# Kernel tuning notes

Hardware: AMD Instinct MI355X
Metric: run time of the kernel (lower is better)

The kernel has to match this reference:

```python
import jax, jax.numpy as jnp
import numpy as np

B = 2048   # batch size
D = 2048   # feature dim (ResNet-50)
H = 2048   # projection hidden dim
T = 0.1    # temperature
EPS_BN = 1e-5
CC_ITERS = 32  # >= ~2*log2(B), enough for pointer-jumping convergence


def setup_inputs() -> dict:
    key = jax.random.key(0)
    ks = jax.random.split(key, 4)
    s = 0.02
    return {
        "x1": jax.random.normal(ks[0], (B, D), dtype=jnp.float32),
        "x2": jax.random.normal(ks[1], (B, D), dtype=jnp.float32),
        "W1": jax.random.normal(ks[2], (H, D), dtype=jnp.float32) * s,
        "b1": jnp.zeros((H,), jnp.float32),
        "gamma": jnp.ones((H,), jnp.float32),
        "beta": jnp.zeros((H,), jnp.float32),
        "W2": jax.random.normal(ks[3], (D, H), dtype=jnp.float32) * s,
        "b2": jnp.zeros((D,), jnp.float32),
    }


def _head(x, W1, b1, gamma, beta, W2, b2):
    # ProjectionHead: Linear -> BatchNorm1d (train mode, batch stats) -> ReLU -> Linear
    h = x @ W1.T + b1
    mu = h.mean(0)
    var = h.var(0)  # biased variance, as torch BN uses for normalization
    h = (h - mu) * jax.lax.rsqrt(var + EPS_BN) * gamma + beta
    h = jax.nn.relu(h)
    o = h @ W2.T + b2
    n = jnp.maximum(jnp.linalg.norm(o, axis=1, keepdims=True), 1e-12)
    return o / n  # F.normalize


def _cc_mask(feat):
    # build_connected_component: kNN(k=1) graph + connected components -> same-label mask
    b = feat.shape[0]
    sim = jax.lax.stop_gradient(feat @ feat.T) - 2.0 * jnp.eye(b, dtype=feat.dtype)
    y = jnp.argmax(sim, axis=1)  # topk(1) neighbor per row
    # min-label propagation with pointer jumping (GPU-native union-find equivalent)
    def body(_, l):
        ln = jnp.minimum(l, l[y])      # propagate along edge i -> y[i]
        ln = ln.at[y].min(l)           # propagate along reverse edge y[i] -> i
        return jnp.minimum(ln, ln[ln])  # pointer jumping
    labels = jax.lax.fori_loop(0, CC_ITERS, body, jnp.arange(b))
    return (labels[:, None] == labels[None, :]).astype(feat.dtype)


def _sup_contra(logits, mask, diag):
    dm = 1.0 - diag
    mask = mask * dm
    exp_logits = jnp.exp(logits) * dm
    log_prob = logits - jnp.log(exp_logits.sum(1, keepdims=True))
    mean_log_prob_pos = (mask * log_prob).sum(1) / mask.sum(1)
    return (-mean_log_prob_pos).mean()


def reference(x1, x2, W1, b1, gamma, beta, W2, b2):
    # Only head2 branch contributes to the returned graph_loss (head1 branch is dead code
    # w.r.t. the return value), so we compute exactly the graph_loss path.
    feat1 = _head(x1, W1, b1, gamma, beta, W2, b2)
    feat2 = _head(x2, W1, b1, gamma, beta, W2, b2)
    mask1 = _cc_mask(feat1)
    mask2 = _cc_mask(feat2)
    diag = jnp.eye(B, dtype=feat1.dtype)
    loss = _sup_contra(feat1 @ feat1.T / T, mask2, diag)
    loss = loss + _sup_contra(feat2 @ feat2.T / T, mask1, diag)
    return loss / 2.0
```

## Files before the change

### kernel.cpp

```cpp
#include <hip/hip_runtime.h>
#include <hip/hip_bf16.h>

typedef __bf16 bf16_t;
typedef __bf16 bf16x4 __attribute__((ext_vector_type(4)));
typedef __bf16 bf16x8 __attribute__((ext_vector_type(8)));
typedef float  f32x4  __attribute__((ext_vector_type(4)));

__device__ __forceinline__ void gload_lds16(const void* g, void* l)
{
    __builtin_amdgcn_global_load_lds((__attribute__((address_space(1))) void*)g,
                                     (__attribute__((address_space(3))) void*)l,
                                     16, 0, 0);
}

__global__ __launch_bounds__(256) void cast_all(const float* __restrict__ x1, const float* __restrict__ x2,
                                                const float* __restrict__ W1, const float* __restrict__ W2,
                                                bf16_t* __restrict__ xcatb, bf16_t* __restrict__ W1b,
                                                bf16_t* __restrict__ W2b)
{
    const size_t i  = ((size_t)blockIdx.x * 256 + threadIdx.x) * 4;
    const size_t M4 = 1ull << 22;
    const size_t r  = i >> 22;
    const size_t off = i & (M4 - 1);
    const float* src; bf16_t* dst;
    if (r == 0)      { src = x1; dst = xcatb; }
    else if (r == 1) { src = x2; dst = xcatb + M4; }
    else if (r == 2) { src = W1; dst = W1b; }
    else             { src = W2; dst = W2b; }
    f32x4 v = *(const f32x4*)(src + off);
    bf16x4 o;
    o[0] = (bf16_t)v[0]; o[1] = (bf16_t)v[1]; o[2] = (bf16_t)v[2]; o[3] = (bf16_t)v[3];
    *(bf16x4*)(dst + off) = o;
}

__global__ __launch_bounds__(256) void gemm_bt(
    const bf16_t* __restrict__ A, const bf16_t* __restrict__ B,
    const float* __restrict__ bias, void* __restrict__ Cv,
    int N, int K, int rows_per_batch, long long b_batch_stride,
    int mode, int c_bf16,
    float* __restrict__ ps, float* __restrict__ ps2,
    float* __restrict__ rsq, const float* __restrict__ rnv,
    unsigned long long* __restrict__ pkey)
{
    __shared__ bf16_t lsA[128 * 64];
    __shared__ bf16_t lsB[128 * 64];
    __shared__ float  cs2[4][64];
    __shared__ float  cq2[4][64];
    __shared__ float  rq2[4][64];
    __shared__ unsigned long long kv2[4][64];
    const int tid  = threadIdx.x;
    const int lane = tid & 63;
    const int wave = tid >> 6;
    const int wm   = (wave >> 1) * 64;
    const int wn   = (wave & 1) * 64;
    const int m0   = blockIdx.y * 128;
    const int n0   = blockIdx.x * 128;
    const bf16_t* Bb = B + (long long)(m0 / rows_per_batch) * b_batch_stride;

    f32x4 acc[4][4] = {};

    const int srow = tid >> 3;
    const int scol = (tid & 7) * 8;
    for (int kt = 0; kt < K; kt += 64) {
#pragma unroll
        for (int i = 0; i < 4; ++i) {
            const int r = i * 32 + srow;
            gload_lds16(A  + (size_t)(m0 + r) * K + kt + scol, lsA + r * 64 + scol);
            gload_lds16(Bb + (size_t)(n0 + r) * K + kt + scol, lsB + r * 64 + scol);
        }
        __syncthreads();
#pragma unroll
        for (int ks = 0; ks < 2; ++ks) {
            const int kk = ks * 32 + (lane >> 4) * 8;
            bf16x8 af[4], bfr[4];
#pragma unroll
            for (int f = 0; f < 4; ++f) {
                af[f]  = *(const bf16x8*)&lsA[(wm + f * 16 + (lane & 15)) * 64 + kk];
                bfr[f] = *(const bf16x8*)&lsB[(wn + f * 16 + (lane & 15)) * 64 + kk];
            }
#pragma unroll
            for (int fm = 0; fm < 4; ++fm)
#pragma unroll
                for (int fn = 0; fn < 4; ++fn)
                    acc[fm][fn] = __builtin_amdgcn_mfma_f32_16x16x32_bf16(af[fm], bfr[fn], acc[fm][fn], 0, 0, 0);
        }
        __syncthreads();
    }

    if (mode == 2) {
        const int rnb = (m0 >> 11) * 2048;
#pragma unroll
        for (int fm = 0; fm < 4; ++fm) {
            const int mb = m0 + wm + fm * 16 + ((lane >> 4) << 2);
            const f32x4 rm = *(const f32x4*)&rnv[mb];
#pragma unroll
            for (int fn = 0; fn < 4; ++fn) {
                const float rc = rnv[rnb + n0 + wn + fn * 16 + (lane & 15)];
#pragma unroll
                for (int r = 0; r < 4; ++r)
                    acc[fm][fn][r] *= rm[r] * rc;
            }
        }
    }

#pragma unroll
    for (int fm = 0; fm < 4; ++fm) {
        const int rb = m0 + wm + fm * 16 + ((lane >> 4) << 2);
#pragma unroll
        for (int fn = 0; fn < 4; ++fn) {
            const int colg = n0 + wn + fn * 16 + (lane & 15);
            const float bv = bias ? bias[colg] : 0.0f;
            if (c_bf16) {
                bf16_t* Cb = (bf16_t*)Cv;
#pragma unroll
                for (int r = 0; r < 4; ++r)
                    Cb[(size_t)(rb + r) * N + colg] = (bf16_t)(acc[fm][fn][r] + bv);
            } else {
                float* Cf = (float*)Cv;
#pragma unroll
                for (int r = 0; r < 4; ++r)
                    Cf[(size_t)(rb + r) * N + colg] = acc[fm][fn][r] + bv;
            }
        }
    }

    if (mode == 1) {
#pragma unroll
        for (int fn = 0; fn < 4; ++fn) {
            const int cl = fn * 16 + (lane & 15);
            const float bv = bias[n0 + wn + cl];
            float s = 0.f, q = 0.f;
#pragma unroll
            for (int fm = 0; fm < 4; ++fm)
#pragma unroll
                for (int r = 0; r < 4; ++r) {
                    const float v = acc[fm][fn][r] + bv;
                    s += v; q += v * v;
                }
            s += __shfl_xor(s, 16); q += __shfl_xor(q, 16);
            s += __shfl_xor(s, 32); q += __shfl_xor(q, 32);
            if (lane < 16) { cs2[wave][cl] = s; cq2[wave][cl] = q; }
        }
        __syncthreads();
        if (tid < 128) {
            const int wlo = (tid < 64) ? 0 : 1;
            const int cl  = tid & 63;
            ps [(size_t)blockIdx.y * 2048 + n0 + tid] = cs2[wlo][cl] + cs2[wlo + 2][cl];
            ps2[(size_t)blockIdx.y * 2048 + n0 + tid] = cq2[wlo][cl] + cq2[wlo + 2][cl];
        }
    } else if (mode == 3) {
#pragma unroll
        for (int fm = 0; fm < 4; ++fm)
#pragma unroll
            for (int r = 0; r < 4; ++r) {
                float q = 0.f;
#pragma unroll
                for (int fn = 0; fn < 4; ++fn) {
                    const float v = acc[fm][fn][r] + bias[n0 + wn + fn * 16 + (lane & 15)];
                    q += v * v;
                }
                q += __shfl_xor(q, 1); q += __shfl_xor(q, 2);
                q += __shfl_xor(q, 4); q += __shfl_xor(q, 8);
                if ((lane & 15) == 0)
                    rq2[wave][fm * 16 + ((lane >> 4) << 2) + r] = q;
            }
        __syncthreads();
        if (tid < 128) {
            const int wlo = (tid < 64) ? 0 : 2;
            const int rl  = tid & 63;
            rsq[(size_t)blockIdx.x * 4096 + m0 + tid] = rq2[wlo][rl] + rq2[wlo + 1][rl];
        }
    } else if (mode == 2) {
#pragma unroll
        for (int fm = 0; fm < 4; ++fm)
#pragma unroll
            for (int r = 0; r < 4; ++r) {
                const int rl   = fm * 16 + ((lane >> 4) << 2) + r;
                const int self = (m0 + wm + rl) & 2047;
                float best = -1.0e38f; int bi = 0x7fffffff;
#pragma unroll
                for (int fn = 0; fn < 4; ++fn) {
                    const int cg = n0 + wn + fn * 16 + (lane & 15);
                    const float v = acc[fm][fn][r];
                    if (cg != self && v > best) { best = v; bi = cg; }
                }
#pragma unroll
                for (int st = 1; st <= 8; st <<= 1) {
                    const float ov = __shfl_xor(best, st);
                    const int   oi = __shfl_xor(bi, st);
                    if (ov > best || (ov == best && oi < bi)) { best = ov; bi = oi; }
                }
                if ((lane & 15) == 0) {
                    unsigned u = __float_as_uint(best);
                    u = (u & 0x80000000u) ? ~u : (u | 0x80000000u);
                    kv2[wave][rl] = ((unsigned long long)u << 32) | (unsigned)(~bi);
                }
            }
        __syncthreads();
        if (tid < 128) {
            const int wlo = (tid < 64) ? 0 : 2;
            const int rl  = tid & 63;
            const unsigned long long a = kv2[wlo][rl], b = kv2[wlo + 1][rl];
            pkey[(size_t)blockIdx.x * 4096 + m0 + tid] = a > b ? a : b;
        }
    }
}

__global__ __launch_bounds__(256) void bn_final2(const float* __restrict__ ps, const float* __restrict__ ps2,
                                                 float* __restrict__ mu, float* __restrict__ rinv)
{
    const int c = blockIdx.x * 256 + threadIdx.x;
    const int b = c >> 11, col = c & 2047;
    float s = 0.f, s2 = 0.f;
    for (int i = 0; i < 16; ++i) {
        s  += ps [(size_t)(b * 16 + i) * 2048 + col];
        s2 += ps2[(size_t)(b * 16 + i) * 2048 + col];
    }
    const float m = s * (1.0f / 2048.0f);
    const float v = s2 * (1.0f / 2048.0f) - m * m;
    mu[c]   = m;
    rinv[c] = rsqrtf(v + 1e-5f);
}

__global__ __launch_bounds__(256) void bn_apply(const bf16_t* __restrict__ h, const float* __restrict__ mu,
                                                const float* __restrict__ rinv, const float* __restrict__ gamma,
                                                const float* __restrict__ beta, bf16_t* __restrict__ out)
{
    const size_t base = ((size_t)blockIdx.x * 256 + threadIdx.x) * 8;
    const int col = (int)(base & 2047);
    const int br  = (int)(base >> 22);
    bf16x8 v = *(const bf16x8*)(h + base);
    bf16x8 o;
#pragma unroll
    for (int j = 0; j < 8; ++j) {
        const int c = col + j;
        const float f = (float)v[j];
        const float t = (f - mu[br * 2048 + c]) * rinv[br * 2048 + c] * gamma[c] + beta[c];
        o[j] = (bf16_t)fmaxf(t, 0.0f);
    }
    *(bf16x8*)(out + base) = o;
}

__global__ __launch_bounds__(256) void norm_final(const float* __restrict__ rsq, float* __restrict__ rn)
{
    const int r = blockIdx.x * 256 + threadIdx.x;
    float s = 0.f;
    for (int nb = 0; nb < 16; ++nb) s += rsq[(size_t)nb * 4096 + r];
    rn[r] = 1.0f / fmaxf(sqrtf(s), 1e-12f);
}

__global__ __launch_bounds__(1024) void cc_labels(const unsigned long long* __restrict__ pkey,
                                                  int* __restrict__ labg)
{
    __shared__ int A_[2048];
    __shared__ int Bn[2048];
    __shared__ int Y_[2048];
    __shared__ int chg;
    const int br = blockIdx.x;
    const int t = threadIdx.x;
    if (t == 0) chg = 0;
    for (int i = t; i < 2048; i += 1024) {
        const int row = br * 2048 + i;
        unsigned long long k = 0ull;
        for (int nb = 0; nb < 16; ++nb) {
            const unsigned long long v = pkey[(size_t)nb * 4096 + row];
            k = (v > k) ? v : k;
        }
        Y_[i] = (int)~((unsigned)(k & 0xFFFFFFFFull));
        A_[i] = i;
    }
    __syncthreads();
    for (int it = 0; it < 32; ++it) {
        for (int i = t; i < 2048; i += 1024) Bn[i] = min(A_[i], A_[Y_[i]]);
        __syncthreads();
        for (int i = t; i < 2048; i += 1024) atomicMin(&Bn[Y_[i]], A_[i]);
        __syncthreads();
        int ch = 0;
        for (int i = t; i < 2048; i += 1024) {
            const int b = Bn[i];
            const int nv = min(b, Bn[b]);
            if (nv != A_[i]) { ch = 1; A_[i] = nv; }
        }
        if (ch) atomicOr(&chg, 1);
        __syncthreads();
        const int c = chg;
        __syncthreads();
        if (t == 0) chg = 0;
        if (!c) break;
    }
    for (int i = t; i < 2048; i += 1024) labg[br * 2048 + i] = A_[i];
}

__global__ __launch_bounds__(256) void loss_rows(const float* __restrict__ sim, const int* __restrict__ labels,
                                                 float* __restrict__ terms)
{
    const int row = blockIdx.x;
    const int br  = row >> 11;
    const int* lab = labels + ((1 - br) << 11);
    const int self = row & 2047;
    const int li = lab[self];
    const int t = threadIdx.x;
    const f32x4* p = (const f32x4*)(sim + (size_t)row * 2048);
    f32x4 a = p[t * 2], b = p[t * 2 + 1];
    float se = 0.f, psum = 0.f; int pc = 0;
#pragma unroll
    for (int j = 0; j < 8; ++j) {
        const int c = t * 8 + j;
        const float v = (j < 4) ? a[j] : b[j - 4];
        if (c == self) continue;
        const float lg = v * 10.0f;
        se += expf(lg);
        if (lab[c] == li) { psum += lg; pc++; }
    }
    __shared__ float SE[256], PS[256]; __shared__ int PC[256];
    SE[t] = se; PS[t] = psum; PC[t] = pc;
    __syncthreads();
    for (int off = 128; off; off >>= 1) {
        if (t < off) { SE[t] += SE[t + off]; PS[t] += PS[t + off]; PC[t] += PC[t + off]; }
        __syncthreads();
    }
    if (t == 0) terms[row] = logf(SE[0]) - PS[0] / (float)PC[0];
}

__global__ __launch_bounds__(1024) void final_reduce(const float* __restrict__ terms, float* __restrict__ out)
{
    const int t = threadIdx.x;
    float s = terms[t] + terms[t + 1024] + terms[t + 2048] + terms[t + 3072];
    __shared__ float S[1024];
    S[t] = s;
    __syncthreads();
    for (int off = 512; off; off >>= 1) { if (t < off) S[t] += S[t + off]; __syncthreads(); }
    if (t == 0) out[0] = S[0] * (1.0f / 4096.0f);
}

extern "C" void kernel_launch(void* const* d_in, const int* in_sizes, int n_in,
                              void* d_out, int out_size, void* d_ws, size_t ws_size,
                              hipStream_t stream)
{
    const float* x1    = (const float*)d_in[0];
    const float* x2    = (const float*)d_in[1];
    const float* W1    = (const float*)d_in[2];
    const float* b1    = (const float*)d_in[3];
    const float* gamma = (const float*)d_in[4];
    const float* beta  = (const float*)d_in[5];
    const float* W2    = (const float*)d_in[6];
    const float* b2    = (const float*)d_in[7];

    char* ws = (char*)d_ws;
    const size_t MB = 1024ull * 1024ull;
    const size_t NN = 2048ull * 2048ull;
    bf16_t* W1b    = (bf16_t*)(ws + 0);
    bf16_t* W2b    = (bf16_t*)(ws + 8 * MB);
    bf16_t* xcatb  = (bf16_t*)(ws + 16 * MB);
    bf16_t* hnb    = (bf16_t*)(ws + 16 * MB);
    bf16_t* hb16   = (bf16_t*)(ws + 32 * MB);
    bf16_t* ob16   = (bf16_t*)(ws + 64 * MB);
    float*  sim    = (float*)(ws + 0);
    float*  psA    = (float*)(ws + 80 * MB);
    float*  psB    = psA + 32 * 2048;
    float*  rsq    = psB + 32 * 2048;
    float*  mu     = rsq + 16 * 4096;
    float*  rinv   = mu + 4096;
    float*  rn     = rinv + 4096;
    unsigned long long* pkey = (unsigned long long*)(rn + 4096);
    int*    labels = (int*)(pkey + 16 * 4096);
    float*  terms  = (float*)(labels + 4096);

    cast_all<<<16384, 256, 0, stream>>>(x1, x2, W1, W2, xcatb, W1b, W2b);

    gemm_bt<<<dim3(16, 32), 256, 0, stream>>>(xcatb, W1b, b1, hb16, 2048, 2048, 1 << 30, 0,
                                              1, 1, psA, psB, nullptr, nullptr, nullptr);
    bn_final2<<<16, 256, 0, stream>>>(psA, psB, mu, rinv);
    bn_apply<<<4096, 256, 0, stream>>>(hb16, mu, rinv, gamma, beta, hnb);

    gemm_bt<<<dim3(16, 32), 256, 0, stream>>>(hnb, W2b, b2, ob16, 2048, 2048, 1 << 30, 0,
                                              3, 1, nullptr, nullptr, rsq, nullptr, nullptr);
    norm_final<<<16, 256, 0, stream>>>(rsq, rn);

    gemm_bt<<<dim3(16, 32), 256, 0, stream>>>(ob16, ob16, nullptr, sim, 2048, 2048, 2048, (long long)NN,
                                              2, 0, nullptr, nullptr, nullptr, rn, pkey);

    cc_labels<<<2, 1024, 0, stream>>>(pkey, labels);
    loss_rows<<<4096, 256, 0, stream>>>(sim, labels, terms);
    final_reduce<<<1, 1024, 0, stream>>>(terms, (float*)d_out);
}
```

Measured before the change: 231.4 us.

## Use 8-wave GEMM tiles, fuse softmax exp-sum into sim GEMM, store sim as bf16

The GEMM now runs 512 threads (8 waves, each owning a 64x32 subtile) on the same 128x128 block tile, so each wave holds fewer accumulators. The similarity GEMM epilogue now computes per-row partial sums of exp(10*sim) alongside the argmax and writes them to a new partial buffer. Because of that, the sim matrix can be stored in bf16 and loss_rows only reads it for the positive-mask sum, which halves that matrix's memory traffic. The exp-sum is computed from fp32 accumulators, but the positive log-prob sum now reads bf16-rounded values, which slightly lowers precision.

```diff
diff --git a/kernel.cpp b/kernel.cpp
--- a/kernel.cpp
+++ b/kernel.cpp
@@ -33,38 +33,39 @@
     *(bf16x4*)(dst + off) = o;
 }
 
-__global__ __launch_bounds__(256) void gemm_bt(
+__global__ __launch_bounds__(512, 4) void gemm_bt(
     const bf16_t* __restrict__ A, const bf16_t* __restrict__ B,
     const float* __restrict__ bias, void* __restrict__ Cv,
     int N, int K, int rows_per_batch, long long b_batch_stride,
     int mode, int c_bf16,
     float* __restrict__ ps, float* __restrict__ ps2,
     float* __restrict__ rsq, const float* __restrict__ rnv,
-    unsigned long long* __restrict__ pkey)
+    unsigned long long* __restrict__ pkey, float* __restrict__ lseP)
 {
     __shared__ bf16_t lsA[128 * 64];
     __shared__ bf16_t lsB[128 * 64];
-    __shared__ float  cs2[4][64];
-    __shared__ float  cq2[4][64];
-    __shared__ float  rq2[4][64];
-    __shared__ unsigned long long kv2[4][64];
+    __shared__ float  cs2[8][32];
+    __shared__ float  cq2[8][32];
+    __shared__ float  rq2[8][64];
+    __shared__ float  ls2[8][64];
+    __shared__ unsigned long long kv2[8][64];
     const int tid  = threadIdx.x;
     const int lane = tid & 63;
     const int wave = tid >> 6;
-    const int wm   = (wave >> 1) * 64;
-    const int wn   = (wave & 1) * 64;
+    const int wm   = (wave >> 2) * 64;
+    const int wn   = (wave & 3) * 32;
     const int m0   = blockIdx.y * 128;
     const int n0   = blockIdx.x * 128;
     const bf16_t* Bb = B + (long long)(m0 / rows_per_batch) * b_batch_stride;
 
-    f32x4 acc[4][4] = {};
+    f32x4 acc[4][2] = {};
 
     const int srow = tid >> 3;
     const int scol = (tid & 7) * 8;
     for (int kt = 0; kt < K; kt += 64) {
 #pragma unroll
-        for (int i = 0; i < 4; ++i) {
-            const int r = i * 32 + srow;
+        for (int i = 0; i < 2; ++i) {
+            const int r = i * 64 + srow;
             gload_lds16(A  + (size_t)(m0 + r) * K + kt + scol, lsA + r * 64 + scol);
             gload_lds16(Bb + (size_t)(n0 + r) * K + kt + scol, lsB + r * 64 + scol);
         }
@@ -72,16 +73,17 @@
 #pragma unroll
         for (int ks = 0; ks < 2; ++ks) {
             const int kk = ks * 32 + (lane >> 4) * 8;
-            bf16x8 af[4], bfr[4];
-#pragma unroll
-            for (int f = 0; f < 4; ++f) {
+            bf16x8 af[4], bfr[2];
+#pragma unroll
+            for (int f = 0; f < 4; ++f)
                 af[f]  = *(const bf16x8*)&lsA[(wm + f * 16 + (lane & 15)) * 64 + kk];
-                bfr[f] = *(const bf16x8*)&lsB[(wn + f * 16 + (lane & 15)) * 64 + kk];
-            }
+#pragma unroll
+            for (int g = 0; g < 2; ++g)
+                bfr[g] = *(const bf16x8*)&lsB[(wn + g * 16 + (lane & 15)) * 64 + kk];
 #pragma unroll
             for (int fm = 0; fm < 4; ++fm)
 #pragma unroll
-                for (int fn = 0; fn < 4; ++fn)
+                for (int fn = 0; fn < 2; ++fn)
                     acc[fm][fn] = __builtin_amdgcn_mfma_f32_16x16x32_bf16(af[fm], bfr[fn], acc[fm][fn], 0, 0, 0);
         }
         __syncthreads();
@@ -94,7 +96,7 @@
             const int mb = m0 + wm + fm * 16 + ((lane >> 4) << 2);
             const f32x4 rm = *(const f32x4*)&rnv[mb];
 #pragma unroll
-            for (int fn = 0; fn < 4; ++fn) {
+            for (int fn = 0; fn < 2; ++fn) {
                 const float rc = rnv[rnb + n0 + wn + fn * 16 + (lane & 15)];
 #pragma unroll
                 for (int r = 0; r < 4; ++r)
@@ -107,7 +109,7 @@
     for (int fm = 0; fm < 4; ++fm) {
         const int rb = m0 + wm + fm * 16 + ((lane >> 4) << 2);
 #pragma unroll
-        for (int fn = 0; fn < 4; ++fn) {
+        for (int fn = 0; fn < 2; ++fn) {
             const int colg = n0 + wn + fn * 16 + (lane & 15);
             const float bv = bias ? bias[colg] : 0.0f;
             if (c_bf16) {
@@ -126,9 +128,9 @@
 
     if (mode == 1) {
 #pragma unroll
-        for (int fn = 0; fn < 4; ++fn) {
-            const int cl = fn * 16 + (lane & 15);
-            const float bv = bias[n0 + wn + cl];
+        for (int fn = 0; fn < 2; ++fn) {
+            const int cl32 = fn * 16 + (lane & 15);
+            const float bv = bias[n0 + wn + cl32];
             float s = 0.f, q = 0.f;
 #pragma unroll
             for (int fm = 0; fm < 4; ++fm)
@@ -139,14 +141,13 @@
                 }
             s += __shfl_xor(s, 16); q += __shfl_xor(q, 16);
             s += __shfl_xor(s, 32); q += __shfl_xor(q, 32);
-            if (lane < 16) { cs2[wave][cl] = s; cq2[wave][cl] = q; }
+            if (lane < 16) { cs2[wave][cl32] = s; cq2[wave][cl32] = q; }
         }
         __syncthreads();
         if (tid < 128) {
-            const int wlo = (tid < 64) ? 0 : 1;
-            const int cl  = tid & 63;
-            ps [(size_t)blockIdx.y * 2048 + n0 + tid] = cs2[wlo][cl] + cs2[wlo + 2][cl];
-            ps2[(size_t)blockIdx.y * 2048 + n0 + tid] = cq2[wlo][cl] + cq2[wlo + 2][cl];
+            const int qv = tid >> 5, cl = tid & 31;
+            ps [(size_t)blockIdx.y * 2048 + n0 + tid] = cs2[qv][cl] + cs2[qv + 4][cl];
+            ps2[(size_t)blockIdx.y * 2048 + n0 + tid] = cq2[qv][cl] + cq2[qv + 4][cl];
         }
     } else if (mode == 3) {
 #pragma unroll
@@ -155,7 +156,7 @@
             for (int r = 0; r < 4; ++r) {
                 float q = 0.f;
 #pragma unroll
-                for (int fn = 0; fn < 4; ++fn) {
+                for (int fn = 0; fn < 2; ++fn) {
                     const float v = acc[fm][fn][r] + bias[n0 + wn + fn * 16 + (lane & 15)];
                     q += v * v;
                 }
@@ -166,9 +167,9 @@
             }
         __syncthreads();
         if (tid < 128) {
-            const int wlo = (tid < 64) ? 0 : 2;
-            const int rl  = tid & 63;
-            rsq[(size_t)blockIdx.x * 4096 + m0 + tid] = rq2[wlo][rl] + rq2[wlo + 1][rl];
+            const int wlo = (tid >> 6) * 4, rl = tid & 63;
+            rsq[(size_t)blockIdx.x * 4096 + m0 + tid] =
+                rq2[wlo][rl] + rq2[wlo + 1][rl] + rq2[wlo + 2][rl] + rq2[wlo + 3][rl];
         }
     } else if (mode == 2) {
 #pragma unroll
@@ -177,31 +178,39 @@
             for (int r = 0; r < 4; ++r) {
                 const int rl   = fm * 16 + ((lane >> 4) << 2) + r;
                 const int self = (m0 + wm + rl) & 2047;
-                float best = -1.0e38f; int bi = 0x7fffffff;
-#pragma unroll
-                for (int fn = 0; fn < 4; ++fn) {
+                float best = -1.0e38f; int bi = 0x7fffffff; float se = 0.f;
+#pragma unroll
+                for (int fn = 0; fn < 2; ++fn) {
                     const int cg = n0 + wn + fn * 16 + (lane & 15);
                     const float v = acc[fm][fn][r];
-                    if (cg != self && v > best) { best = v; bi = cg; }
+                    if (cg != self) {
+                        se += expf(10.0f * v);
+                        if (v > best) { best = v; bi = cg; }
+                    }
                 }
 #pragma unroll
                 for (int st = 1; st <= 8; st <<= 1) {
                     const float ov = __shfl_xor(best, st);
                     const int   oi = __shfl_xor(bi, st);
                     if (ov > best || (ov == best && oi < bi)) { best = ov; bi = oi; }
+                    se += __shfl_xor(se, st);
                 }
                 if ((lane & 15) == 0) {
                     unsigned u = __float_as_uint(best);
                     u = (u & 0x80000000u) ? ~u : (u | 0x80000000u);
                     kv2[wave][rl] = ((unsigned long long)u << 32) | (unsigned)(~bi);
+                    ls2[wave][rl] = se;
                 }
             }
         __syncthreads();
         if (tid < 128) {
-            const int wlo = (tid < 64) ? 0 : 2;
-            const int rl  = tid & 63;
-            const unsigned long long a = kv2[wlo][rl], b = kv2[wlo + 1][rl];
-            pkey[(size_t)blockIdx.x * 4096 + m0 + tid] = a > b ? a : b;
+            const int wlo = (tid >> 6) * 4, rl = tid & 63;
+            unsigned long long k = kv2[wlo][rl];
+#pragma unroll
+            for (int j = 1; j < 4; ++j) { const unsigned long long v = kv2[wlo + j][rl]; k = v > k ? v : k; }
+            pkey[(size_t)blockIdx.x * 4096 + m0 + tid] = k;
+            lseP[(size_t)blockIdx.x * 4096 + m0 + tid] =
+                ls2[wlo][rl] + ls2[wlo + 1][rl] + ls2[wlo + 2][rl] + ls2[wlo + 3][rl];
         }
     }
 }
@@ -291,8 +300,8 @@
     for (int i = t; i < 2048; i += 1024) labg[br * 2048 + i] = A_[i];
 }
 
-__global__ __launch_bounds__(256) void loss_rows(const float* __restrict__ sim, const int* __restrict__ labels,
-                                                 float* __restrict__ terms)
+__global__ __launch_bounds__(256) void loss_rows(const bf16_t* __restrict__ simb, const int* __restrict__ labels,
+                                                 const float* __restrict__ lseP, float* __restrict__ terms)
 {
     const int row = blockIdx.x;
     const int br  = row >> 11;
@@ -300,26 +309,26 @@
     const int self = row & 2047;
     const int li = lab[self];
     const int t = threadIdx.x;
-    const f32x4* p = (const f32x4*)(sim + (size_t)row * 2048);
-    f32x4 a = p[t * 2], b = p[t * 2 + 1];
-    float se = 0.f, psum = 0.f; int pc = 0;
+    const bf16x8 v8 = *(const bf16x8*)(simb + (size_t)row * 2048 + t * 8);
+    float psum = 0.f; int pc = 0;
 #pragma unroll
     for (int j = 0; j < 8; ++j) {
         const int c = t * 8 + j;
-        const float v = (j < 4) ? a[j] : b[j - 4];
         if (c == self) continue;
-        const float lg = v * 10.0f;
-        se += expf(lg);
-        if (lab[c] == li) { psum += lg; pc++; }
-    }
-    __shared__ float SE[256], PS[256]; __shared__ int PC[256];
-    SE[t] = se; PS[t] = psum; PC[t] = pc;
+        if (lab[c] == li) { psum += 10.0f * (float)v8[j]; pc++; }
+    }
+    __shared__ float PS[256]; __shared__ int PC[256];
+    PS[t] = psum; PC[t] = pc;
     __syncthreads();
     for (int off = 128; off; off >>= 1) {
-        if (t < off) { SE[t] += SE[t + off]; PS[t] += PS[t + off]; PC[t] += PC[t + off]; }
-        __syncthreads();
-    }
-    if (t == 0) terms[row] = logf(SE[0]) - PS[0] / (float)PC[0];
+        if (t < off) { PS[t] += PS[t + off]; PC[t] += PC[t + off]; }
+        __syncthreads();
+    }
+    if (t == 0) {
+        float se = 0.f;
+        for (int nb = 0; nb < 16; ++nb) se += lseP[(size_t)nb * 4096 + row];
+        terms[row] = logf(se) - PS[0] / (float)PC[0];
+    }
 }
 
 __global__ __launch_bounds__(1024) void final_reduce(const float* __restrict__ terms, float* __restrict__ out)
@@ -355,32 +364,33 @@
     bf16_t* hnb    = (bf16_t*)(ws + 16 * MB);
     bf16_t* hb16   = (bf16_t*)(ws + 32 * MB);
     bf16_t* ob16   = (bf16_t*)(ws + 64 * MB);
-    float*  sim    = (float*)(ws + 0);
+    bf16_t* simb   = (bf16_t*)(ws + 0);
     float*  psA    = (float*)(ws + 80 * MB);
     float*  psB    = psA + 32 * 2048;
     float*  rsq    = psB + 32 * 2048;
     float*  mu     = rsq + 16 * 4096;
     float*  rinv   = mu + 4096;
     float*  rn     = rinv + 4096;
-    unsigned long long* pkey = (unsigned long long*)(rn + 4096);
+    float*  lseP   = rn + 4096;
+    unsigned long long* pkey = (unsigned long long*)(lseP + 16 * 4096);
     int*    labels = (int*)(pkey + 16 * 4096);
     float*  terms  = (float*)(labels + 4096);
 
     cast_all<<<16384, 256, 0, stream>>>(x1, x2, W1, W2, xcatb, W1b, W2b);
 
-    gemm_bt<<<dim3(16, 32), 256, 0, stream>>>(xcatb, W1b, b1, hb16, 2048, 2048, 1 << 30, 0,
-                                              1, 1, psA, psB, nullptr, nullptr, nullptr);
+    gemm_bt<<<dim3(16, 32), 512, 0, stream>>>(xcatb, W1b, b1, hb16, 2048, 2048, 1 << 30, 0,
+                                              1, 1, psA, psB, nullptr, nullptr, nullptr, nullptr);
     bn_final2<<<16, 256, 0, stream>>>(psA, psB, mu, rinv);
     bn_apply<<<4096, 256, 0, stream>>>(hb16, mu, rinv, gamma, beta, hnb);
 
-    gemm_bt<<<dim3(16, 32), 256, 0, stream>>>(hnb, W2b, b2, ob16, 2048, 2048, 1 << 30, 0,
-                                              3, 1, nullptr, nullptr, rsq, nullptr, nullptr);
+    gemm_bt<<<dim3(16, 32), 512, 0, stream>>>(hnb, W2b, b2, ob16, 2048, 2048, 1 << 30, 0,
+                                              3, 1, nullptr, nullptr, rsq, nullptr, nullptr, nullptr);
     norm_final<<<16, 256, 0, stream>>>(rsq, rn);
 
-    gemm_bt<<<dim3(16, 32), 256, 0, stream>>>(ob16, ob16, nullptr, sim, 2048, 2048, 2048, (long long)NN,
-                                              2, 0, nullptr, nullptr, nullptr, rn, pkey);
+    gemm_bt<<<dim3(16, 32), 512, 0, stream>>>(ob16, ob16, nullptr, simb, 2048, 2048, 2048, (long long)NN,
+                                              2, 1, nullptr, nullptr, nullptr, rn, pkey, lseP);
 
     cc_labels<<<2, 1024, 0, stream>>>(pkey, labels);
-    loss_rows<<<4096, 256, 0, stream>>>(sim, labels, terms);
+    loss_rows<<<4096, 256, 0, stream>>>(simb, labels, lseP, terms);
     final_reduce<<<1, 1024, 0, stream>>>(terms, (float*)d_out);
 }
```

After: 236.0 us. Within noise of the previous version (+2.0%).

## Fuse row exp-sum into similarity GEMM epilogue and store similarity as bf16

Applied to the files above, without the earlier changes.

The similarity GEMM epilogue now computes per-tile partial sums of exp(10*sim) for each row (excluding the diagonal) and writes them to a partials buffer. The similarity matrix is stored in bf16 instead of fp32. The loss kernel then only reads bf16 values for the positive-pair sum and combines the 16 exp partials. This halves the similarity write and read traffic and removes the exp work from the loss pass. In exchange the GEMM epilogue gets heavier, and the positive-logit sum loses precision from bf16 rounding.

```diff
diff --git a/kernel.cpp b/kernel.cpp
--- a/kernel.cpp
+++ b/kernel.cpp
@@ -40,13 +40,14 @@
     int mode, int c_bf16,
     float* __restrict__ ps, float* __restrict__ ps2,
     float* __restrict__ rsq, const float* __restrict__ rnv,
-    unsigned long long* __restrict__ pkey)
+    unsigned long long* __restrict__ pkey, float* __restrict__ lseP)
 {
     __shared__ bf16_t lsA[128 * 64];
     __shared__ bf16_t lsB[128 * 64];
     __shared__ float  cs2[4][64];
     __shared__ float  cq2[4][64];
     __shared__ float  rq2[4][64];
+    __shared__ float  ls2[4][64];
     __shared__ unsigned long long kv2[4][64];
     const int tid  = threadIdx.x;
     const int lane = tid & 63;
@@ -177,23 +178,28 @@
             for (int r = 0; r < 4; ++r) {
                 const int rl   = fm * 16 + ((lane >> 4) << 2) + r;
                 const int self = (m0 + wm + rl) & 2047;
-                float best = -1.0e38f; int bi = 0x7fffffff;
+                float best = -1.0e38f; int bi = 0x7fffffff; float se = 0.f;
 #pragma unroll
                 for (int fn = 0; fn < 4; ++fn) {
                     const int cg = n0 + wn + fn * 16 + (lane & 15);
                     const float v = acc[fm][fn][r];
-                    if (cg != self && v > best) { best = v; bi = cg; }
+                    if (cg != self) {
+                        se += expf(10.0f * v);
+                        if (v > best) { best = v; bi = cg; }
+                    }
                 }
 #pragma unroll
                 for (int st = 1; st <= 8; st <<= 1) {
                     const float ov = __shfl_xor(best, st);
                     const int   oi = __shfl_xor(bi, st);
                     if (ov > best || (ov == best && oi < bi)) { best = ov; bi = oi; }
+                    se += __shfl_xor(se, st);
                 }
                 if ((lane & 15) == 0) {
                     unsigned u = __float_as_uint(best);
                     u = (u & 0x80000000u) ? ~u : (u | 0x80000000u);
                     kv2[wave][rl] = ((unsigned long long)u << 32) | (unsigned)(~bi);
+                    ls2[wave][rl] = se;
                 }
             }
         __syncthreads();
@@ -202,6 +208,7 @@
             const int rl  = tid & 63;
             const unsigned long long a = kv2[wlo][rl], b = kv2[wlo + 1][rl];
             pkey[(size_t)blockIdx.x * 4096 + m0 + tid] = a > b ? a : b;
+            lseP[(size_t)blockIdx.x * 4096 + m0 + tid] = ls2[wlo][rl] + ls2[wlo + 1][rl];
         }
     }
 }
@@ -291,8 +298,8 @@
     for (int i = t; i < 2048; i += 1024) labg[br * 2048 + i] = A_[i];
 }
 
-__global__ __launch_bounds__(256) void loss_rows(const float* __restrict__ sim, const int* __restrict__ labels,
-                                                 float* __restrict__ terms)
+__global__ __launch_bounds__(256) void loss_rows(const bf16_t* __restrict__ simb, const int* __restrict__ labels,
+                                                 const float* __restrict__ lseP, float* __restrict__ terms)
 {
     const int row = blockIdx.x;
     const int br  = row >> 11;
@@ -300,26 +307,26 @@
     const int self = row & 2047;
     const int li = lab[self];
     const int t = threadIdx.x;
-    const f32x4* p = (const f32x4*)(sim + (size_t)row * 2048);
-    f32x4 a = p[t * 2], b = p[t * 2 + 1];
-    float se = 0.f, psum = 0.f; int pc = 0;
+    const bf16x8 v8 = *(const bf16x8*)(simb + (size_t)row * 2048 + t * 8);
+    float psum = 0.f; int pc = 0;
 #pragma unroll
     for (int j = 0; j < 8; ++j) {
         const int c = t * 8 + j;
-        const float v = (j < 4) ? a[j] : b[j - 4];
         if (c == self) continue;
-        const float lg = v * 10.0f;
-        se += expf(lg);
-        if (lab[c] == li) { psum += lg; pc++; }
-    }
-    __shared__ float SE[256], PS[256]; __shared__ int PC[256];
-    SE[t] = se; PS[t] = psum; PC[t] = pc;
+        if (lab[c] == li) { psum += 10.0f * (float)v8[j]; pc++; }
+    }
+    __shared__ float PS[256]; __shared__ int PC[256];
+    PS[t] = psum; PC[t] = pc;
     __syncthreads();
     for (int off = 128; off; off >>= 1) {
-        if (t < off) { SE[t] += SE[t + off]; PS[t] += PS[t + off]; PC[t] += PC[t + off]; }
-        __syncthreads();
-    }
-    if (t == 0) terms[row] = logf(SE[0]) - PS[0] / (float)PC[0];
+        if (t < off) { PS[t] += PS[t + off]; PC[t] += PC[t + off]; }
+        __syncthreads();
+    }
+    if (t == 0) {
+        float se = 0.f;
+        for (int nb = 0; nb < 16; ++nb) se += lseP[(size_t)nb * 4096 + row];
+        terms[row] = logf(se) - PS[0] / (float)PC[0];
+    }
 }
 
 __global__ __launch_bounds__(1024) void final_reduce(const float* __restrict__ terms, float* __restrict__ out)
@@ -355,32 +362,33 @@
     bf16_t* hnb    = (bf16_t*)(ws + 16 * MB);
     bf16_t* hb16   = (bf16_t*)(ws + 32 * MB);
     bf16_t* ob16   = (bf16_t*)(ws + 64 * MB);
-    float*  sim    = (float*)(ws + 0);
+    bf16_t* simb   = (bf16_t*)(ws + 0);
     float*  psA    = (float*)(ws + 80 * MB);
     float*  psB    = psA + 32 * 2048;
     float*  rsq    = psB + 32 * 2048;
     float*  mu     = rsq + 16 * 4096;
     float*  rinv   = mu + 4096;
     float*  rn     = rinv + 4096;
-    unsigned long long* pkey = (unsigned long long*)(rn + 4096);
+    float*  lseP   = rn + 4096;
+    unsigned long long* pkey = (unsigned long long*)(lseP + 16 * 4096);
     int*    labels = (int*)(pkey + 16 * 4096);
     float*  terms  = (float*)(labels + 4096);
 
     cast_all<<<16384, 256, 0, stream>>>(x1, x2, W1, W2, xcatb, W1b, W2b);
 
     gemm_bt<<<dim3(16, 32), 256, 0, stream>>>(xcatb, W1b, b1, hb16, 2048, 2048, 1 << 30, 0,
-                                              1, 1, psA, psB, nullptr, nullptr, nullptr);
+                                              1, 1, psA, psB, nullptr, nullptr, nullptr, nullptr);
     bn_final2<<<16, 256, 0, stream>>>(psA, psB, mu, rinv);
     bn_apply<<<4096, 256, 0, stream>>>(hb16, mu, rinv, gamma, beta, hnb);
 
     gemm_bt<<<dim3(16, 32), 256, 0, stream>>>(hnb, W2b, b2, ob16, 2048, 2048, 1 << 30, 0,
-                                              3, 1, nullptr, nullptr, rsq, nullptr, nullptr);
+                                              3, 1, nullptr, nullptr, rsq, nullptr, nullptr, nullptr);
     norm_final<<<16, 256, 0, stream>>>(rsq, rn);
 
-    gemm_bt<<<dim3(16, 32), 256, 0, stream>>>(ob16, ob16, nullptr, sim, 2048, 2048, 2048, (long long)NN,
-                                              2, 0, nullptr, nullptr, nullptr, rn, pkey);
+    gemm_bt<<<dim3(16, 32), 256, 0, stream>>>(ob16, ob16, nullptr, simb, 2048, 2048, 2048, (long long)NN,
+                                              2, 1, nullptr, nullptr, nullptr, rn, pkey, lseP);
 
     cc_labels<<<2, 1024, 0, stream>>>(pkey, labels);
-    loss_rows<<<4096, 256, 0, stream>>>(sim, labels, terms);
+    loss_rows<<<4096, 256, 0, stream>>>(simb, labels, lseP, terms);
     final_reduce<<<1, 1024, 0, stream>>>(terms, (float*)d_out);
 }
```

Result: slower. 238.8 us (+3.2%).
